# Optimization experiments

Measured on AMD Instinct MI355X. Metric: run time of the kernel, lower is better.

The kernel has to match this reference:

```python
import jax, jax.numpy as jnp
import numpy as np

B, DIM, X, Y = 8, 256, 1, 4096
H, D = 8, 64            # heads, dim_head
INNER = H * D           # 512
K0 = K1 = 4
SCALE = D ** -0.5


def setup_inputs() -> dict:
    key = jax.random.key(0)
    ks = jax.random.split(key, 10)
    s_in = 1.0 / np.sqrt(DIM)
    s_kv = 1.0 / np.sqrt(DIM * K0 * K0)
    s_out = 1.0 / np.sqrt(INNER)
    return {
        "x0": jax.random.normal(ks[0], (B, DIM, X, Y), jnp.float32),
        "x1": jax.random.normal(ks[1], (B, DIM, X, Y), jnp.float32),
        "Wq0": jax.random.normal(ks[2], (INNER, DIM), jnp.float32) * s_in,
        "Wkv0": jax.random.normal(ks[3], (2 * INNER, DIM, K0, K0), jnp.float32) * s_kv,
        "Wq1": jax.random.normal(ks[4], (INNER, DIM), jnp.float32) * s_in,
        "Wkv1": jax.random.normal(ks[5], (2 * INNER, DIM, K1, K1), jnp.float32) * s_kv,
        "Wout0": jax.random.normal(ks[6], (DIM, INNER), jnp.float32) * s_out,
        "bout0": jnp.zeros((DIM,), jnp.float32),
        "Wout1": jax.random.normal(ks[7], (DIM, INNER), jnp.float32) * s_out,
        "bout1": jnp.zeros((DIM,), jnp.float32),
    }


def _proj_q(x, W):
    # 1x1 conv: [b, n, 1, y] -> [b, h, y, d]
    b = x.shape[0]
    q = jnp.einsum('on,bnxy->boxy', W, x)          # [b, inner, 1, y]
    return q.reshape(b, H, D, X * Y).transpose(0, 1, 3, 2)


def _proj_kv(x, W, k):
    # patch-window the y axis, then k x k conv with stride k == full patch contraction
    b, n = x.shape[0], x.shape[1]
    w = Y // (k * k)                                # number of KV tokens
    xp = x.reshape(b, n, w, k, k)                   # x-dim (==1) absorbed into w
    kv = jnp.einsum('bnwpq,onpq->bow', xp, W)       # [b, 2*inner, w]
    kk, vv = jnp.split(kv, 2, axis=1)
    kk = kk.reshape(b, H, D, w).transpose(0, 1, 3, 2)   # [b, h, w, d]
    vv = vv.reshape(b, H, D, w).transpose(0, 1, 3, 2)
    return kk, vv


def _attend(q, k, v):
    # q: [b,h,y,d], k/v: [b,h,w,d] -> [b, h*d, 1, y]
    b = q.shape[0]
    dots = jnp.einsum('bhid,bhjd->bhij', q, k) * SCALE
    attn = jax.nn.softmax(dots, axis=-1)
    o = jnp.einsum('bhij,bhjd->bhid', attn, v)
    return o.transpose(0, 1, 3, 2).reshape(b, H * D, X, Y)


def _out_proj(o, W, b_):
    return jnp.einsum('oc,bcxy->boxy', W, o) + b_[None, :, None, None]


def reference(x0, x1, Wq0, Wkv0, Wq1, Wkv1, Wout0, bout0, Wout1, bout1):
    q0 = _proj_q(x0, Wq0)
    k0_, v0_ = _proj_kv(x0, Wkv0, K0)
    q1 = _proj_q(x1, Wq1)
    k1_, v1_ = _proj_kv(x1, Wkv1, K1)
    out0 = _out_proj(_attend(q0, k1_, v1_), Wout0, bout0)
    out1 = _out_proj(_attend(q1, k0_, v0_), Wout1, bout1)
    return 0.5 * ((x1 + out0) + (x0 + out1))
```

## Files before the change

kernel.cpp:

```cpp
#include <hip/hip_runtime.h>
#include <hip/hip_bf16.h>


typedef unsigned short u16;
typedef unsigned int   u32;
typedef __bf16 v8bf __attribute__((ext_vector_type(8)));
typedef float  v4f  __attribute__((ext_vector_type(4)));
typedef u16    v8u  __attribute__((ext_vector_type(8)));

#define MFMA16(a,b,c) __builtin_amdgcn_mfma_f32_16x16x32_bf16((a),(b),(c),0,0,0)

__device__ __forceinline__ u16 f2bf(float f){ union{float f; u32 i;} x; x.f=f; u32 r=x.i+0x7FFFu+((x.i>>16)&1u); return (u16)(r>>16); }

__device__ __forceinline__ v8bf load8f_bf(const float* __restrict__ p){
  union { v8bf v; u16 u[8]; } t;
  float4 a = *(const float4*)p, b = *(const float4*)(p+4);
  t.u[0]=f2bf(a.x); t.u[1]=f2bf(a.y); t.u[2]=f2bf(a.z); t.u[3]=f2bf(a.w);
  t.u[4]=f2bf(b.x); t.u[5]=f2bf(b.y); t.u[6]=f2bf(b.z); t.u[7]=f2bf(b.w);
  return t.v;
}

__device__ __forceinline__ void gld16(u16* lds, const u16* g) {
  __builtin_amdgcn_global_load_lds(
      (const __attribute__((address_space(1))) void*)g,
      (__attribute__((address_space(3))) void*)lds, 16, 0, 0);
}

#define OFF_XPT(s) ((size_t)(s)*8388608u)
#define OFF_Q(s)   ((size_t)16777216u + (size_t)(s)*16777216u)
#define OFF_ATT(s) ((size_t)50331648u + (size_t)(s)*16777216u)
#define OFF_WKV(s) ((size_t)50331648u + (size_t)(s)*4194304u)
#define OFF_K(s)   ((size_t)83886080u + (size_t)(s)*1048576u)
#define OFF_V(s)   ((size_t)85983232u + (size_t)(s)*1048576u)

__global__ __launch_bounds__(256) void pack_kernel(const float* __restrict__ x0,
    const float* __restrict__ x1, u16* __restrict__ ws) {
  const int w = blockIdx.x & 255;
  const int b = (blockIdx.x >> 8) & 7;
  const int s = blockIdx.x >> 11;
  const float* x = s ? x1 : x0;
  const int n = threadIdx.x;
  const float* src = x + ((size_t)(b*256 + n))*4096 + w*16;
  u16* dst = ws + OFF_XPT(s) + ((size_t)(b*256 + w))*4096 + n*16;
  float4 f0 = *(const float4*)(src);
  float4 f1 = *(const float4*)(src+4);
  float4 f2 = *(const float4*)(src+8);
  float4 f3 = *(const float4*)(src+12);
  union { v8u v; u16 u[8]; } lo, hi;
  lo.u[0]=f2bf(f0.x); lo.u[1]=f2bf(f0.y); lo.u[2]=f2bf(f0.z); lo.u[3]=f2bf(f0.w);
  lo.u[4]=f2bf(f1.x); lo.u[5]=f2bf(f1.y); lo.u[6]=f2bf(f1.z); lo.u[7]=f2bf(f1.w);
  hi.u[0]=f2bf(f2.x); hi.u[1]=f2bf(f2.y); hi.u[2]=f2bf(f2.z); hi.u[3]=f2bf(f2.w);
  hi.u[4]=f2bf(f3.x); hi.u[5]=f2bf(f3.y); hi.u[6]=f2bf(f3.z); hi.u[7]=f2bf(f3.w);
  *(v8u*)(dst)   = lo.v;
  *(v8u*)(dst+8) = hi.v;
}

__global__ __launch_bounds__(256) void wconv_kernel(const float* __restrict__ Wkv0,
    const float* __restrict__ Wkv1, u16* __restrict__ ws) {
  int tid = blockIdx.x*256 + threadIdx.x;
  int s = tid >> 19;
  int i8 = tid & 524287;
  const float* W = s ? Wkv1 : Wkv0;
  const float* src = W + (size_t)i8*8;
  u16* dst = ws + OFF_WKV(s) + (size_t)i8*8;
  float4 a = *(const float4*)src, b = *(const float4*)(src+4);
  union { v8u v; u16 u[8]; } t;
  t.u[0]=f2bf(a.x); t.u[1]=f2bf(a.y); t.u[2]=f2bf(a.z); t.u[3]=f2bf(a.w);
  t.u[4]=f2bf(b.x); t.u[5]=f2bf(b.y); t.u[6]=f2bf(b.z); t.u[7]=f2bf(b.w);
  *(v8u*)dst = t.v;
}

__global__ __launch_bounds__(256) void qproj_kernel(const float* __restrict__ x0,
    const float* __restrict__ x1, const float* __restrict__ Wq0,
    const float* __restrict__ Wq1, u16* __restrict__ ws) {
  const int yt = blockIdx.x;
  const int ot = blockIdx.y;
  const int s  = blockIdx.z >> 3, b = blockIdx.z & 7;
  const float* x  = s ? x1 : x0;
  const float* Wq = s ? Wq1 : Wq0;
  u16* qout = ws + OFF_Q(s);
  const int y0 = yt*128, o0 = ot*128;

  __shared__ u16 sm[32768];
  {
    const int tn = threadIdx.x >> 4;
    const int ty = (threadIdx.x & 15) * 8;
    #pragma unroll
    for (int pass = 0; pass < 16; ++pass) {
      int n = pass*16 + tn;
      const float* src = x + ((size_t)(b*256 + n))*4096 + y0 + ty;
      float4 fa = *(const float4*)src, fb = *(const float4*)(src+4);
      u16 vals[8] = { f2bf(fa.x), f2bf(fa.y), f2bf(fa.z), f2bf(fa.w),
                      f2bf(fb.x), f2bf(fb.y), f2bf(fb.z), f2bf(fb.w) };
      #pragma unroll
      for (int j = 0; j < 8; ++j) {
        int row = ty + j;
        int byte = row*512 + ((2*n) ^ (j<<4));
        sm[byte>>1] = vals[j];
      }
    }
  }
  __syncthreads();

  const int lane = threadIdx.x & 63, wv = threadIdx.x >> 6;
  const int l16 = lane & 15, g = lane >> 4;
  const int wm = wv >> 1, wn = wv & 1;

  v4f acc[4][4] = {};
  #pragma unroll
  for (int ks = 0; ks < 8; ++ks) {
    v8bf a[4], bb[4];
    #pragma unroll
    for (int mt = 0; mt < 4; ++mt)
      a[mt] = load8f_bf(Wq + (size_t)(o0 + wm*64 + mt*16 + l16)*256 + ks*32 + g*8);
    #pragma unroll
    for (int nt = 0; nt < 4; ++nt) {
      int row = wn*64 + nt*16 + l16;
      int c = ks*4 + g;
      int byte = row*512 + ((c*16) ^ ((row&7)<<4));
      bb[nt] = *(const v8bf*)&sm[byte>>1];
    }
    #pragma unroll
    for (int mt = 0; mt < 4; ++mt)
      #pragma unroll
      for (int nt = 0; nt < 4; ++nt)
        acc[mt][nt] = MFMA16(a[mt], bb[nt], acc[mt][nt]);
  }
  #pragma unroll
  for (int mt = 0; mt < 4; ++mt)
    #pragma unroll
    for (int nt = 0; nt < 4; ++nt)
      #pragma unroll
      for (int r = 0; r < 4; ++r) {
        int o = o0 + wm*64 + mt*16 + g*4 + r;
        int y = y0 + wn*64 + nt*16 + l16;
        qout[(size_t)(b*512 + o)*4096 + y] = f2bf(acc[mt][nt][r]);
      }
}

__global__ __launch_bounds__(256) void kvproj_kernel(const u16* __restrict__ ws,
                                                     float* __restrict__ part) {
  const int mt8 = blockIdx.x;
  const int nt  = blockIdx.y;
  const int z   = blockIdx.z;
  const int s = z >> 1, kh = z & 1;
  const u16* A = ws + OFF_WKV(s);
  const u16* Bm = ws + OFF_XPT(s);
  const int m0 = mt8*128, n0 = nt*128, kbase = kh*2048;

  __shared__ u16 smA[8192];
  __shared__ u16 smB[8192];

  const int t = threadIdx.x;
  const int trow = t >> 3, tu = t & 7;
  const int cswz = ((tu ^ (trow & 7)) * 8);
  const u16* Asrc = A  + (size_t)(m0 + trow)*4096 + kbase + cswz;
  const u16* Bsrc = Bm + (size_t)(n0 + trow)*4096 + kbase + cswz;
  u16* Adst = smA + t*8;
  u16* Bdst = smB + t*8;

  const int lane = t & 63, wv = t >> 6;
  const int l16 = lane & 15, g = lane >> 4;
  const int wm = wv >> 1, wn = wv & 1;
  const int swz = l16 & 7;

  v4f acc[4][4] = {};
  for (int k0 = 0; k0 < 2048; k0 += 64) {
    #pragma unroll
    for (int i = 0; i < 4; ++i) {
      gld16(Adst + i*2048, Asrc + k0 + (size_t)i*32*4096);
      gld16(Bdst + i*2048, Bsrc + k0 + (size_t)i*32*4096);
    }
    __syncthreads();
    #pragma unroll
    for (int ks = 0; ks < 2; ++ks) {
      v8bf a[4], bb[4];
      #pragma unroll
      for (int mt = 0; mt < 4; ++mt) {
        int row = wm*64 + mt*16 + l16;
        a[mt] = *(const v8bf*)&smA[row*64 + (((ks*4+g) ^ swz)<<3)];
      }
      #pragma unroll
      for (int ntf = 0; ntf < 4; ++ntf) {
        int row = wn*64 + ntf*16 + l16;
        bb[ntf] = *(const v8bf*)&smB[row*64 + (((ks*4+g) ^ swz)<<3)];
      }
      #pragma unroll
      for (int mt = 0; mt < 4; ++mt)
        #pragma unroll
        for (int ntf = 0; ntf < 4; ++ntf)
          acc[mt][ntf] = MFMA16(a[mt], bb[ntf], acc[mt][ntf]);
    }
    __syncthreads();
  }

  float* p = part + ((size_t)z*1024 + m0)*2048 + n0;
  #pragma unroll
  for (int mt = 0; mt < 4; ++mt)
    #pragma unroll
    for (int ntf = 0; ntf < 4; ++ntf)
      #pragma unroll
      for (int r = 0; r < 4; ++r) {
        int row = wm*64 + mt*16 + g*4 + r;
        int col = wn*64 + ntf*16 + l16;
        p[(size_t)row*2048 + col] = acc[mt][ntf][r];
      }
}

__global__ __launch_bounds__(256) void kvreduce_kernel(const float* __restrict__ part,
                                                       u16* __restrict__ ws) {
  int tid = blockIdx.x*256 + threadIdx.x;
  int n8 = tid & 255;
  int o  = (tid >> 8) & 1023;
  int s  = tid >> 18;
  const float* p0 = part + (((size_t)(s*2+0)*1024 + o)*2048) + n8*8;
  const float* p1 = part + (((size_t)(s*2+1)*1024 + o)*2048) + n8*8;
  float4 a0 = *(const float4*)p0, a1 = *(const float4*)(p0+4);
  float4 b0 = *(const float4*)p1, b1 = *(const float4*)(p1+4);
  float v0 = a0.x+b0.x, v1 = a0.y+b0.y, v2 = a0.z+b0.z, v3 = a0.w+b0.w;
  float v4 = a1.x+b1.x, v5 = a1.y+b1.y, v6 = a1.z+b1.z, v7 = a1.w+b1.w;
  int n = n8*8;
  int b = n >> 8, w0 = n & 255;
  if (o < 512) {
    int hh = o >> 6, d = o & 63;
    u16* kout = ws + OFF_K(s) + ((size_t)(b*8+hh)*256)*64 + d;
    kout[(w0+0)*64] = f2bf(v0); kout[(w0+1)*64] = f2bf(v1);
    kout[(w0+2)*64] = f2bf(v2); kout[(w0+3)*64] = f2bf(v3);
    kout[(w0+4)*64] = f2bf(v4); kout[(w0+5)*64] = f2bf(v5);
    kout[(w0+6)*64] = f2bf(v6); kout[(w0+7)*64] = f2bf(v7);
  } else {
    int oo = o - 512, hh = oo >> 6, d = oo & 63;
    union { v8u v; u16 u[8]; } t;
    t.u[0]=f2bf(v0); t.u[1]=f2bf(v1); t.u[2]=f2bf(v2); t.u[3]=f2bf(v3);
    t.u[4]=f2bf(v4); t.u[5]=f2bf(v5); t.u[6]=f2bf(v6); t.u[7]=f2bf(v7);
    *(v8u*)(ws + OFF_V(s) + ((size_t)(b*8+hh)*64 + d)*256 + w0) = t.v;
  }
}

__global__ __launch_bounds__(256) void attn_kernel(u16* __restrict__ ws) {
  const int it = blockIdx.x;
  const int hh = blockIdx.y;
  const int s  = blockIdx.z >> 3, b = blockIdx.z & 7;
  const u16* q  = ws + OFF_Q(s);
  const u16* kk = ws + OFF_K(1-s);
  const u16* vv = ws + OFF_V(1-s);
  u16* att = ws + OFF_ATT(s);

  __shared__ u16 sm[32768];
  const int lane = threadIdx.x & 63, wv = threadIdx.x >> 6;
  const int l16 = lane & 15, g = lane >> 4;

  const u16* kbase = kk + (size_t)(b*8+hh)*16384;
  #pragma unroll
  for (int pass = 0; pass < 8; ++pass) {
    int byte = pass*4096 + threadIdx.x*16;
    int row = byte >> 7, u = (byte >> 4) & 7;
    v8u val = *(const v8u*)(kbase + row*64 + u*8);
    int db = row*128 + ((u*16) ^ ((row&7)<<4));
    *(v8u*)&sm[db>>1] = val;
  }
  const u16* vbase = vv + (size_t)(b*8+hh)*16384;
  #pragma unroll
  for (int pass = 0; pass < 8; ++pass) {
    int byte = pass*4096 + threadIdx.x*16;
    int row = byte >> 9, u = (byte >> 4) & 31;
    v8u val = *(const v8u*)(vbase + row*256 + u*8);
    int db = 32768 + row*512 + ((u*16) ^ ((row&7)<<4));
    *(v8u*)&sm[db>>1] = val;
  }
  __syncthreads();

  const int i0 = it*64 + wv*16;
  v8bf aq[2];
  {
    union { v8bf v; u16 u[8]; } tmp;
    #pragma unroll
    for (int half = 0; half < 2; ++half) {
      #pragma unroll
      for (int jj = 0; jj < 8; ++jj) {
        int d = half*32 + g*8 + jj;
        tmp.u[jj] = q[((size_t)(b*512) + hh*64 + d)*4096 + i0 + l16];
      }
      aq[half] = tmp.v;
    }
  }
  v4f sfr[16];
  #pragma unroll
  for (int t = 0; t < 16; ++t) {
    v4f acc = {};
    #pragma unroll
    for (int half = 0; half < 2; ++half) {
      int row = t*16 + l16;
      int c = half*4 + g;
      int byte = row*128 + ((c*16) ^ ((row&7)<<4));
      v8bf bk = *(const v8bf*)&sm[byte>>1];
      acc = MFMA16(aq[half], bk, acc);
    }
    sfr[t] = acc;
  }
  float inv4[4];
  #pragma unroll
  for (int r = 0; r < 4; ++r) {
    float m = -3.0e38f;
    #pragma unroll
    for (int t = 0; t < 16; ++t) m = fmaxf(m, sfr[t][r]);
    #pragma unroll
    for (int off = 1; off < 16; off <<= 1) m = fmaxf(m, __shfl_xor(m, off));
    float sum = 0.f;
    #pragma unroll
    for (int t = 0; t < 16; ++t) {
      float p = exp2f((sfr[t][r] - m) * 0.18033688011112042f);
      sfr[t][r] = p;
      sum += p;
    }
    #pragma unroll
    for (int off = 1; off < 16; off <<= 1) sum += __shfl_xor(sum, off);
    inv4[r] = 1.0f / sum;
  }
  __syncthreads();
  const int pbase = wv*8192;
  #pragma unroll
  for (int t = 0; t < 16; ++t)
    #pragma unroll
    for (int r = 0; r < 4; ++r) {
      int irow = g*4 + r;
      int j = t*16 + l16;
      int byte = pbase + irow*512 + ((2*j) ^ ((irow&7)<<4));
      sm[byte>>1] = f2bf(sfr[t][r] * inv4[r]);
    }
  __syncthreads();
  v4f oacc[4] = {};
  #pragma unroll
  for (int ksj = 0; ksj < 8; ++ksj) {
    int cp = ksj*4 + g;
    int pbyte = pbase + l16*512 + ((cp*16) ^ ((l16&7)<<4));
    v8bf pa = *(const v8bf*)&sm[pbyte>>1];
    #pragma unroll
    for (int dt = 0; dt < 4; ++dt) {
      int rowv = dt*16 + l16;
      int byte = 32768 + rowv*512 + ((cp*16) ^ ((rowv&7)<<4));
      v8bf vb = *(const v8bf*)&sm[byte>>1];
      oacc[dt] = MFMA16(pa, vb, oacc[dt]);
    }
  }
  #pragma unroll
  for (int dt = 0; dt < 4; ++dt)
    #pragma unroll
    for (int r = 0; r < 4; ++r) {
      int i = i0 + g*4 + r;
      int c = hh*64 + dt*16 + l16;
      att[((size_t)(b*4096) + i)*512 + c] = f2bf(oacc[dt][r]);
    }
}

__global__ __launch_bounds__(256) void outproj_kernel(const float* __restrict__ x0,
    const float* __restrict__ x1, const float* __restrict__ Wout0,
    const float* __restrict__ Wout1, const float* __restrict__ bout0,
    const float* __restrict__ bout1, const u16* __restrict__ ws,
    float* __restrict__ out) {
  const int yt = blockIdx.x;
  const int ot = blockIdx.y;
  const int b  = blockIdx.z;
  const int lane = threadIdx.x & 63, wv = threadIdx.x >> 6;
  const int l16 = lane & 15, g = lane >> 4;
  const int wm = wv >> 1, wn = wv & 1;
  const int y0 = yt*128, o0 = ot*128;

  v4f acc[4][4] = {};
  #pragma unroll
  for (int s = 0; s < 2; ++s) {
    const float* Wout = s ? Wout1 : Wout0;
    const u16* att = ws + OFF_ATT(s);
    #pragma unroll
    for (int ks = 0; ks < 16; ++ks) {
      v8bf a[4], bb[4];
      #pragma unroll
      for (int mt = 0; mt < 4; ++mt)
        a[mt] = load8f_bf(Wout + (size_t)(o0 + wm*64 + mt*16 + l16)*512 + ks*32 + g*8);
      #pragma unroll
      for (int nt = 0; nt < 4; ++nt)
        bb[nt] = *(const v8bf*)(att + ((size_t)(b*4096) + y0 + wn*64 + nt*16 + l16)*512 + ks*32 + g*8);
      #pragma unroll
      for (int mt = 0; mt < 4; ++mt)
        #pragma unroll
        for (int nt = 0; nt < 4; ++nt)
          acc[mt][nt] = MFMA16(a[mt], bb[nt], acc[mt][nt]);
    }
  }
  #pragma unroll
  for (int mt = 0; mt < 4; ++mt)
    #pragma unroll
    for (int nt = 0; nt < 4; ++nt)
      #pragma unroll
      for (int r = 0; r < 4; ++r) {
        int o = o0 + wm*64 + mt*16 + g*4 + r;
        int y = y0 + wn*64 + nt*16 + l16;
        size_t idx = (size_t)(b*256 + o)*4096 + y;
        float bias = bout0[o] + bout1[o];
        out[idx] = 0.5f*(acc[mt][nt][r] + bias + x0[idx] + x1[idx]);
      }
}

extern "C" void kernel_launch(void* const* d_in, const int* in_sizes, int n_in,
                              void* d_out, int out_size, void* d_ws, size_t ws_size,
                              hipStream_t stream) {
  const float* x0    = (const float*)d_in[0];
  const float* x1    = (const float*)d_in[1];
  const float* Wq0   = (const float*)d_in[2];
  const float* Wkv0  = (const float*)d_in[3];
  const float* Wq1   = (const float*)d_in[4];
  const float* Wkv1  = (const float*)d_in[5];
  const float* Wout0 = (const float*)d_in[6];
  const float* bout0 = (const float*)d_in[7];
  const float* Wout1 = (const float*)d_in[8];
  const float* bout1 = (const float*)d_in[9];
  u16*   ws   = (u16*)d_ws;
  float* part = (float*)(ws + OFF_ATT(1));
  float* out  = (float*)d_out;

  pack_kernel    <<<4096, 256, 0, stream>>>(x0, x1, ws);
  wconv_kernel   <<<4096, 256, 0, stream>>>(Wkv0, Wkv1, ws);
  qproj_kernel   <<<dim3(32,4,16), 256, 0, stream>>>(x0, x1, Wq0, Wq1, ws);
  kvproj_kernel  <<<dim3(8,16,4),  256, 0, stream>>>(ws, part);
  kvreduce_kernel<<<2048, 256, 0, stream>>>(part, ws);
  attn_kernel    <<<dim3(64,8,16), 256, 0, stream>>>(ws);
  outproj_kernel <<<dim3(32,2,8),  256, 0, stream>>>(x0, x1, Wout0, Wout1,
                                                     bout0, bout1, ws, out);
}
```

Measured before the change: 549.2 us.

## Loop attention blocks over several query tiles and reuse V in LDS

Each attention block now processes four 64-row query tiles instead of one, so the grid shrinks fourfold and the V tile is loaded into LDS once per block via global_load_lds. K is reloaded each iteration because the probability buffer overlaps its LDS region. To let P be written as packed vector stores, the KV projection permutes the token order of the V half so it matches a transposed P column layout. The softmax also uses an FMA-based exponent, hardware reciprocal, packed bf16 conversion, and defers normalization to the output. The trade-off is fewer blocks for latency hiding, repeated K loads, and a layout coupling between kvproj and attention that is easy to break.

```diff
diff --git a/kernel.cpp b/kernel.cpp
--- a/kernel.cpp
+++ b/kernel.cpp
@@ -7,10 +7,16 @@
 typedef __bf16 v8bf __attribute__((ext_vector_type(8)));
 typedef float  v4f  __attribute__((ext_vector_type(4)));
 typedef u16    v8u  __attribute__((ext_vector_type(8)));
+typedef u32    v4u32 __attribute__((ext_vector_type(4)));
 
 #define MFMA16(a,b,c) __builtin_amdgcn_mfma_f32_16x16x32_bf16((a),(b),(c),0,0,0)
 
 __device__ __forceinline__ u16 f2bf(float f){ union{float f; u32 i;} x; x.f=f; u32 r=x.i+0x7FFFu+((x.i>>16)&1u); return (u16)(r>>16); }
+
+__device__ __forceinline__ u32 cvtpk(float lo, float hi){
+  u32 r; asm("v_cvt_pk_bf16_f32 %0, %1, %2" : "=v"(r) : "v"(lo), "v"(hi));
+  return r;
+}
 
 __device__ __forceinline__ v8bf load8f_bf(const float* __restrict__ p){
   union { v8bf v; u16 u[8]; } t;
@@ -194,16 +200,20 @@
     __syncthreads();
   }
 
-  float* p = part + ((size_t)z*1024 + m0)*2048 + n0;
+  float* pz = part + (size_t)z*1024*2048;
   #pragma unroll
   for (int mt = 0; mt < 4; ++mt)
     #pragma unroll
     for (int ntf = 0; ntf < 4; ++ntf)
       #pragma unroll
       for (int r = 0; r < 4; ++r) {
-        int row = wm*64 + mt*16 + g*4 + r;
-        int col = wn*64 + ntf*16 + l16;
-        p[(size_t)row*2048 + col] = acc[mt][ntf][r];
+        int row = m0 + wm*64 + mt*16 + g*4 + r;
+        int col = n0 + wn*64 + ntf*16 + l16;
+        if (mt8 >= 4) {
+          int cw = col & 255;
+          col = (col & ~255) | (((cw & 15) << 4) | (cw >> 4));
+        }
+        pz[(size_t)row*2048 + col] = acc[mt][ntf][r];
       }
 }
 
@@ -237,8 +247,9 @@
   }
 }
 
+#define ATT_IT 4
 __global__ __launch_bounds__(256) void attn_kernel(u16* __restrict__ ws) {
-  const int it = blockIdx.x;
+  const int it0 = blockIdx.x * ATT_IT;
   const int hh = blockIdx.y;
   const int s  = blockIdx.z >> 3, b = blockIdx.z & 7;
   const u16* q  = ws + OFF_Q(s);
@@ -247,110 +258,121 @@
   u16* att = ws + OFF_ATT(s);
 
   __shared__ u16 sm[32768];
-  const int lane = threadIdx.x & 63, wv = threadIdx.x >> 6;
+  const int t = threadIdx.x;
+  const int lane = t & 63, wv = t >> 6;
   const int l16 = lane & 15, g = lane >> 4;
 
   const u16* kbase = kk + (size_t)(b*8+hh)*16384;
+  const u16* vbase = vv + (size_t)(b*8+hh)*16384;
+
   #pragma unroll
   for (int pass = 0; pass < 8; ++pass) {
-    int byte = pass*4096 + threadIdx.x*16;
-    int row = byte >> 7, u = (byte >> 4) & 7;
-    v8u val = *(const v8u*)(kbase + row*64 + u*8);
-    int db = row*128 + ((u*16) ^ ((row&7)<<4));
-    *(v8u*)&sm[db>>1] = val;
-  }
-  const u16* vbase = vv + (size_t)(b*8+hh)*16384;
-  #pragma unroll
-  for (int pass = 0; pass < 8; ++pass) {
-    int byte = pass*4096 + threadIdx.x*16;
-    int row = byte >> 9, u = (byte >> 4) & 31;
-    v8u val = *(const v8u*)(vbase + row*256 + u*8);
-    int db = 32768 + row*512 + ((u*16) ^ ((row&7)<<4));
-    *(v8u*)&sm[db>>1] = val;
-  }
-  __syncthreads();
-
-  const int i0 = it*64 + wv*16;
-  v8bf aq[2];
-  {
-    union { v8bf v; u16 u[8]; } tmp;
-    #pragma unroll
-    for (int half = 0; half < 2; ++half) {
-      #pragma unroll
-      for (int jj = 0; jj < 8; ++jj) {
-        int d = half*32 + g*8 + jj;
-        tmp.u[jj] = q[((size_t)(b*512) + hh*64 + d)*4096 + i0 + l16];
-      }
-      aq[half] = tmp.v;
-    }
-  }
-  v4f sfr[16];
-  #pragma unroll
-  for (int t = 0; t < 16; ++t) {
-    v4f acc = {};
-    #pragma unroll
-    for (int half = 0; half < 2; ++half) {
-      int row = t*16 + l16;
-      int c = half*4 + g;
-      int byte = row*128 + ((c*16) ^ ((row&7)<<4));
-      v8bf bk = *(const v8bf*)&sm[byte>>1];
-      acc = MFMA16(aq[half], bk, acc);
-    }
-    sfr[t] = acc;
-  }
-  float inv4[4];
-  #pragma unroll
-  for (int r = 0; r < 4; ++r) {
-    float m = -3.0e38f;
-    #pragma unroll
-    for (int t = 0; t < 16; ++t) m = fmaxf(m, sfr[t][r]);
-    #pragma unroll
-    for (int off = 1; off < 16; off <<= 1) m = fmaxf(m, __shfl_xor(m, off));
-    float sum = 0.f;
-    #pragma unroll
-    for (int t = 0; t < 16; ++t) {
-      float p = exp2f((sfr[t][r] - m) * 0.18033688011112042f);
-      sfr[t][r] = p;
-      sum += p;
-    }
-    #pragma unroll
-    for (int off = 1; off < 16; off <<= 1) sum += __shfl_xor(sum, off);
-    inv4[r] = 1.0f / sum;
-  }
-  __syncthreads();
+    int db = pass*4096 + t*16;
+    int d = db >> 9;
+    int u = ((db >> 4) & 31) ^ (d & 7);
+    gld16(sm + 16384 + (db>>1), vbase + d*256 + u*8);
+  }
+
+  const float C = 0.18033688011112042f;
   const int pbase = wv*8192;
-  #pragma unroll
-  for (int t = 0; t < 16; ++t)
+
+  for (int iter = 0; iter < ATT_IT; ++iter) {
+    const int i0 = (it0 + iter)*64 + wv*16;
+    __syncthreads();
+    #pragma unroll
+    for (int pass = 0; pass < 8; ++pass) {
+      int db = pass*4096 + t*16;
+      int row = db >> 7;
+      int u = ((db >> 4) & 7) ^ (row & 7);
+      gld16(sm + (db>>1), kbase + row*64 + u*8);
+    }
+    v8bf aq[2];
+    {
+      union { v8bf v; u16 u[8]; } tmp;
+      #pragma unroll
+      for (int half = 0; half < 2; ++half) {
+        #pragma unroll
+        for (int jj = 0; jj < 8; ++jj) {
+          int d = half*32 + g*8 + jj;
+          tmp.u[jj] = q[((size_t)(b*512) + hh*64 + d)*4096 + i0 + l16];
+        }
+        aq[half] = tmp.v;
+      }
+    }
+    __syncthreads();
+
+    v4f sfr[16];
+    #pragma unroll
+    for (int tt = 0; tt < 16; ++tt) {
+      v4f acc = {};
+      #pragma unroll
+      for (int half = 0; half < 2; ++half) {
+        int row = tt*16 + l16;
+        int c = half*4 + g;
+        int byte = row*128 + ((c*16) ^ ((row&7)<<4));
+        v8bf bk = *(const v8bf*)&sm[byte>>1];
+        acc = MFMA16(aq[half], bk, acc);
+      }
+      sfr[tt] = acc;
+    }
+    float inv4[4];
     #pragma unroll
     for (int r = 0; r < 4; ++r) {
-      int irow = g*4 + r;
-      int j = t*16 + l16;
-      int byte = pbase + irow*512 + ((2*j) ^ ((irow&7)<<4));
-      sm[byte>>1] = f2bf(sfr[t][r] * inv4[r]);
-    }
-  __syncthreads();
-  v4f oacc[4] = {};
-  #pragma unroll
-  for (int ksj = 0; ksj < 8; ++ksj) {
-    int cp = ksj*4 + g;
-    int pbyte = pbase + l16*512 + ((cp*16) ^ ((l16&7)<<4));
-    v8bf pa = *(const v8bf*)&sm[pbyte>>1];
-    #pragma unroll
-    for (int dt = 0; dt < 4; ++dt) {
-      int rowv = dt*16 + l16;
-      int byte = 32768 + rowv*512 + ((cp*16) ^ ((rowv&7)<<4));
-      v8bf vb = *(const v8bf*)&sm[byte>>1];
-      oacc[dt] = MFMA16(pa, vb, oacc[dt]);
-    }
-  }
-  #pragma unroll
-  for (int dt = 0; dt < 4; ++dt)
+      float m = sfr[0][r];
+      #pragma unroll
+      for (int tt = 1; tt < 16; ++tt) m = fmaxf(m, sfr[tt][r]);
+      #pragma unroll
+      for (int off = 1; off < 16; off <<= 1) m = fmaxf(m, __shfl_xor(m, off));
+      float mc = m * C;
+      float sum = 0.f;
+      #pragma unroll
+      for (int tt = 0; tt < 16; ++tt) {
+        float p = exp2f(fmaf(sfr[tt][r], C, -mc));
+        sfr[tt][r] = p;
+        sum += p;
+      }
+      #pragma unroll
+      for (int off = 1; off < 16; off <<= 1) sum += __shfl_xor(sum, off);
+      inv4[r] = __builtin_amdgcn_rcpf(sum);
+    }
+    __syncthreads();
+
     #pragma unroll
     for (int r = 0; r < 4; ++r) {
-      int i = i0 + g*4 + r;
-      int c = hh*64 + dt*16 + l16;
-      att[((size_t)(b*4096) + i)*512 + c] = f2bf(oacc[dt][r]);
-    }
+      int i = g*4 + r;
+      #pragma unroll
+      for (int half = 0; half < 2; ++half) {
+        v4u32 pk;
+        pk.x = cvtpk(sfr[half*8+0][r], sfr[half*8+1][r]);
+        pk.y = cvtpk(sfr[half*8+2][r], sfr[half*8+3][r]);
+        pk.z = cvtpk(sfr[half*8+4][r], sfr[half*8+5][r]);
+        pk.w = cvtpk(sfr[half*8+6][r], sfr[half*8+7][r]);
+        int byte = pbase + i*512 + ((l16*32 + half*16) ^ ((i&7)<<4));
+        *(v4u32*)&sm[byte>>1] = pk;
+      }
+    }
+    v4f oacc[4] = {};
+    #pragma unroll
+    for (int ksj = 0; ksj < 8; ++ksj) {
+      int pbyte = pbase + l16*512 + (((ksj*4+g)<<4) ^ ((l16&7)<<4));
+      v8bf pa = *(const v8bf*)&sm[pbyte>>1];
+      #pragma unroll
+      for (int dt = 0; dt < 4; ++dt) {
+        int rowv = dt*16 + l16;
+        int byte = 32768 + rowv*512 + (((ksj*4+g)<<4) ^ ((rowv&7)<<4));
+        v8bf vb = *(const v8bf*)&sm[byte>>1];
+        oacc[dt] = MFMA16(pa, vb, oacc[dt]);
+      }
+    }
+    #pragma unroll
+    for (int dt = 0; dt < 4; ++dt)
+      #pragma unroll
+      for (int r = 0; r < 4; ++r) {
+        int i = i0 + g*4 + r;
+        int c = hh*64 + dt*16 + l16;
+        att[((size_t)(b*4096) + i)*512 + c] = f2bf(oacc[dt][r] * inv4[r]);
+      }
+  }
 }
 
 __global__ __launch_bounds__(256) void outproj_kernel(const float* __restrict__ x0,
@@ -423,7 +445,7 @@
   qproj_kernel   <<<dim3(32,4,16), 256, 0, stream>>>(x0, x1, Wq0, Wq1, ws);
   kvproj_kernel  <<<dim3(8,16,4),  256, 0, stream>>>(ws, part);
   kvreduce_kernel<<<2048, 256, 0, stream>>>(part, ws);
-  attn_kernel    <<<dim3(64,8,16), 256, 0, stream>>>(ws);
+  attn_kernel    <<<dim3(16,8,16), 256, 0, stream>>>(ws);
   outproj_kernel <<<dim3(32,2,8),  256, 0, stream>>>(x0, x1, Wout0, Wout1,
                                                      bout0, bout1, ws, out);
 }
```

New measurement: 582.1 us. 1.06x slower.
